# Kernel optimization log

Measured on AMD Instinct MI355X. Metric: run time of the kernel, lower is better.

## Reference

```python
import jax, jax.numpy as jnp
import numpy as np

BIT = 64
N_CLASS = 100
NUM_TRAIN = 100000
BATCH = 512
MU = 1.0   # config['mu']
M = 1.0    # config['m']
ETA = 0.5  # config['eta']
VUL = 1.0  # config['vul']
NTA = 1.0  # config['nta']


def setup_inputs() -> dict:
    key = jax.random.key(0)
    k1, k2, k3, k4, k5, k6 = jax.random.split(key, 6)
    u = jax.random.normal(k1, (BATCH, BIT), jnp.float32)
    # y / Y are one-hot label matrices in DFH; build realistic one-hot floats
    labels = jax.random.randint(k2, (BATCH,), 0, N_CLASS)
    y = jax.nn.one_hot(labels, N_CLASS, dtype=jnp.float32)
    ind = jax.random.randint(k3, (BATCH,), 0, NUM_TRAIN)
    U = jax.random.normal(k4, (BIT, NUM_TRAIN), jnp.float32)
    train_labels = jax.random.randint(k5, (NUM_TRAIN,), 0, N_CLASS)
    Y = jax.nn.one_hot(train_labels, N_CLASS, dtype=jnp.float32).T  # [n_class, num_train]
    V = jax.random.normal(k6, (BIT, N_CLASS), jnp.float32)
    return {"u": u, "y": y, "ind": ind, "U": U, "Y": Y, "V": V}


def _center_gradient(V, y, b):
    # 200-step gradient descent on V minimizing intra + vul*inter + nta*quant.
    n_class = V.shape[1]
    TK = V.shape[0] * (2.0 * jnp.eye(n_class, dtype=V.dtype)
                       - jnp.ones((n_class, n_class), V.dtype))
    yt = y.T  # [n_class, batch]

    def inner_loss(Vc):
        intra = jnp.mean((Vc @ yt - b) ** 2)
        inter = jnp.mean((Vc.T @ Vc - TK) ** 2)
        quant = jnp.mean((Vc - jnp.sign(Vc)) ** 2)
        return intra + VUL * inter + NTA * quant

    grad_fn = jax.grad(inner_loss)

    def step(Vc, i):
        # torch code multiplies alpha by 0.1 *before* the update at i==149 and i==179
        alpha = 0.03 * jnp.where(i >= 149, 0.1, 1.0) * jnp.where(i >= 179, 0.1, 1.0)
        return Vc - alpha * grad_fn(Vc), None

    V_new, _ = jax.lax.scan(step, V, jnp.arange(200))
    return V_new


def reference(u, y, ind, U, Y, V):
    # state buffer updates (torch: self.U[:, ind] = u.t().data, etc.)
    U = U.at[:, ind].set(u.T)
    Y = Y.at[:, ind].set(y.T)
    C = jnp.sign(V)
    b = jnp.sign(MU * (C @ y.T) + u.T)                     # [bit, batch]
    V_new = _center_gradient(V, y, b)                      # updated self.V
    s = (y @ Y > 0).astype(u.dtype)                        # [batch, num_train]
    ip = jnp.clip(0.5 * (u @ U), -100.0, 50.0)             # [batch, num_train]
    metric_loss = jnp.mean((1.0 - s) * jnp.log1p(jnp.exp(M + ip))
                           + s * jnp.log1p(jnp.exp(M - ip)))
    quantization_loss = jnp.mean((b - u.T) ** 2)
    loss = metric_loss + ETA * quantization_loss
    return loss, V_new
```

## Files before the change

kernel.cpp:

```cpp
#include <hip/hip_runtime.h>

#define BIT 64
#define NCLASS 100
#define NTRAIN 100000
#define BATCH 512

#define O_OWNER   0
#define O_TLAB    100000
#define O_LAB     200000
#define O_BMAT    200512
#define O_BSUM    233280
#define O_COUNT   239680
#define O_QSUM    239780
#define O_MSUM    239782

typedef __attribute__((ext_vector_type(8))) short short8v;
typedef __attribute__((ext_vector_type(4))) float f32x4;
typedef unsigned short ushortT;

__device__ __forceinline__ float signf(float x) {
    return (x > 0.f) ? 1.f : ((x < 0.f) ? -1.f : 0.f);
}

__device__ __forceinline__ ushortT f2bf(float x) {
    union { float f; unsigned u; } v; v.f = x;
    unsigned r = v.u + 0x7FFFu + ((v.u >> 16) & 1u);
    return (ushortT)(r >> 16);
}
__device__ __forceinline__ unsigned pk2(float a, float b) {
    return (unsigned)f2bf(a) | ((unsigned)f2bf(b) << 16);
}

__global__ void k_prep(const float* __restrict__ y, const int* __restrict__ ind,
                       int* owner, int* lab) {
    int b = threadIdx.x;
    const float* row = y + b * NCLASS;
    int best = 0;
    for (int c = 0; c < NCLASS; ++c)
        if (row[c] > 0.5f) best = c;
    lab[b] = best;
    atomicMax(&owner[ind[b]], b);
}

__global__ void k_tlab(const float* __restrict__ Y, const int* __restrict__ owner,
                       const int* __restrict__ lab, int* tlab) {
    int j = blockIdx.x * blockDim.x + threadIdx.x;
    if (j >= NTRAIN) return;
    int tl = 0;
    for (int c = 0; c < NCLASS; ++c)
        if (Y[(size_t)c * NTRAIN + j] > 0.5f) tl = c;
    int ow = owner[j];
    tlab[j] = (ow >= 0) ? lab[ow] : tl;
}

__global__ void k_b(const float* __restrict__ u, const float* __restrict__ V,
                    const int* __restrict__ lab, float* bmat, double* qsum) {
    int bb = threadIdx.x;
    int r  = blockIdx.x;
    int c = lab[bb];
    float v  = V[r * NCLASS + c];
    float uu = u[bb * BIT + r];
    float t  = signf(v) + uu;
    float bv = signf(t);
    bmat[r * BATCH + bb] = bv;
    float d = bv - uu;
    double q = (double)(d * d);
    for (int off = 32; off; off >>= 1) q += __shfl_down(q, off);
    __shared__ double wsum[8];
    int wid = threadIdx.x >> 6, lane = threadIdx.x & 63;
    if (lane == 0) wsum[wid] = q;
    __syncthreads();
    if (threadIdx.x == 0) {
        double s = 0;
        for (int w = 0; w < 8; ++w) s += wsum[w];
        atomicAdd(qsum, s);
    }
}

__global__ void k_bsum(const float* __restrict__ bmat, const int* __restrict__ lab,
                       float* Bsum, float* count) {
    __shared__ int slab[BATCH];
    for (int i = threadIdx.x; i < BATCH; i += blockDim.x) slab[i] = lab[i];
    __syncthreads();
    int idx = blockIdx.x * blockDim.x + threadIdx.x;
    if (idx < BIT * NCLASS) {
        int r = idx / NCLASS, c = idx % NCLASS;
        const float* br = bmat + r * BATCH;
        float s = 0.f;
        for (int bb = 0; bb < BATCH; ++bb)
            if (slab[bb] == c) s += br[bb];
        Bsum[idx] = s;
    }
    if (blockIdx.x == 0 && threadIdx.x < NCLASS) {
        int c = threadIdx.x, n = 0;
        for (int bb = 0; bb < BATCH; ++bb)
            if (slab[bb] == c) ++n;
        count[c] = (float)n;
    }
}

__global__ __launch_bounds__(512, 4) void k_main(
        const float* __restrict__ V, const float* __restrict__ Bsum,
        const float* __restrict__ count, const float* __restrict__ u,
        const float* __restrict__ U, const int* __restrict__ lab,
        const int* __restrict__ tlab, const int* __restrict__ owner,
        double* msum, float* __restrict__ out) {
    __shared__ __align__(16) char smem[69888];

    if (blockIdx.x == 0) {
        ushortT* SAb = (ushortT*)smem;
        ushortT* SBb = (ushortT*)(smem + 32768);
        ushortT* SMf = (ushortT*)(smem + 61440);
        float*   rs  = (float*)(smem + 69632);

        const int t = threadIdx.x, l = t & 63, w = t >> 6;
        const int g = l >> 4, c16 = l & 15;
        const short8v ONES = {0x3F80,0x3F80,0x3F80,0x3F80,
                              0x3F80,0x3F80,0x3F80,0x3F80};

        for (int i = t; i < 16384; i += 512) SAb[i] = 0;
        for (int i = t; i < 14336; i += 512) SBb[i] = 0;

        const float ci = 2.0f / 32768.0f;
        const float ce = 4.0f / 10000.0f;
        const float cq = 2.0f / 6400.0f;
        const float ce64 = 64.0f * ce;

        const int mtile = w & 3;
        const int m = mtile * 16 + c16;
        bool wact[4], live[4];
        int ntile[4], saO[4], sbO[4];
        float vreg[4][4], Kc[4][4], ncib[4][4];
        #pragma unroll
        for (int q = 0; q < 4; ++q) {
            const int tp = w + 8 * q;
            wact[q] = (tp < 28);
            const int nt = wact[q] ? (tp >> 2) : 0;
            ntile[q] = nt;
            const int n0 = nt * 16 + 4 * g;
            live[q] = wact[q] && (n0 < NCLASS);
            saO[q] = ((mtile * 4 + (nt >> 1)) * 64 + l) * 8 + 4 * (nt & 1);
            sbO[q] = ((nt * 2 + (mtile >> 1)) * 64 + (4 * g + 16 * (c16 >> 2))) * 8
                     + (c16 & 3) + 4 * (mtile & 1);
            #pragma unroll
            for (int r = 0; r < 4; ++r) {
                float v = 0.f, bs = 0.f, cn = 0.f;
                if (live[q]) {
                    const int n = n0 + r;
                    v  = V[m * NCLASS + n];
                    bs = Bsum[m * NCLASS + n];
                    cn = count[n];
                }
                vreg[q][r] = v;
                Kc[q][r]   = ci * cn + cq - 128.f * ce;
                ncib[q][r] = -ci * bs;
            }
        }

        const int mi_m = w >> 1, mj0 = (w & 1) * 2, mj1 = mj0 + 1;
        const bool dg = (mi_m == mj0) || (mi_m == mj1);
        const int smO0 = ((mj0 * 2 + (mi_m >> 1)) * 64 + l) * 8 + 4 * (mi_m & 1);
        const int smO1 = ((mj1 * 2 + (mi_m >> 1)) * 64 + l) * 8 + 4 * (mi_m & 1);

        __syncthreads();

        #pragma unroll
        for (int q = 0; q < 4; ++q) if (wact[q]) {
            *(uint2*)&SAb[saO[q]] =
                make_uint2(pk2(vreg[q][0], vreg[q][1]), pk2(vreg[q][2], vreg[q][3]));
            #pragma unroll
            for (int r = 0; r < 4; ++r) SBb[sbO[q] + r * 8] = f2bf(vreg[q][r]);
        }
        __syncthreads();

        int cur = 0;
        for (int step = 0; step < 200; ++step) {
            float alpha = 0.03f;
            if (step >= 149) alpha *= 0.1f;
            if (step >= 179) alpha *= 0.1f;

            const ushortT* SAc = SAb + cur * 8192;

            f32x4 aM0 = {0.f,0.f,0.f,0.f}, aM1 = {0.f,0.f,0.f,0.f};
            f32x4 aR  = {0.f,0.f,0.f,0.f};
            #pragma unroll
            for (int ks = 0; ks < 4; ++ks) {
                short8v a  = *(const short8v*)&SAc[((mi_m * 4 + ks) * 64 + l) * 8];
                short8v b0 = *(const short8v*)&SAc[((mj0 * 4 + ks) * 64 + l) * 8];
                short8v b1 = *(const short8v*)&SAc[((mj1 * 4 + ks) * 64 + l) * 8];
                aM0 = __builtin_amdgcn_mfma_f32_16x16x32_bf16(a, b0, aM0, 0, 0, 0);
                aM1 = __builtin_amdgcn_mfma_f32_16x16x32_bf16(a, b1, aM1, 0, 0, 0);
                if (dg)
                    aR = __builtin_amdgcn_mfma_f32_16x16x32_bf16(a, ONES, aR, 0, 0, 0);
            }
            *(uint2*)&SMf[smO0] = make_uint2(pk2(aM0[0], aM0[1]), pk2(aM0[2], aM0[3]));
            *(uint2*)&SMf[smO1] = make_uint2(pk2(aM1[0], aM1[1]), pk2(aM1[2], aM1[3]));
            if (dg && c16 == 0)
                *(f32x4*)&rs[mi_m * 16 + 4 * g] = aR;
            __syncthreads();

            const ushortT* SBc = SBb + cur * 7168;
            f32x4 p[4];
            #pragma unroll
            for (int q = 0; q < 4; ++q) p[q] = (f32x4){0.f,0.f,0.f,0.f};
            #pragma unroll
            for (int kb = 0; kb < 2; ++kb) {
                short8v bP = *(const short8v*)&SMf[((mtile * 2 + kb) * 64 + l) * 8];
                #pragma unroll
                for (int q = 0; q < 4; ++q) if (wact[q]) {
                    short8v aP = *(const short8v*)&SBc[((ntile[q] * 2 + kb) * 64 + l) * 8];
                    p[q] = __builtin_amdgcn_mfma_f32_16x16x32_bf16(aP, bP, p[q], 0, 0, 0);
                }
            }
            const float rsm = rs[m];

            const int nxt = cur ^ 1;
            ushortT* SAn = SAb + nxt * 8192;
            ushortT* SBn = SBb + nxt * 7168;
            #pragma unroll
            for (int q = 0; q < 4; ++q) if (wact[q]) {
                float nv[4];
                #pragma unroll
                for (int r = 0; r < 4; ++r) {
                    const float v = vreg[q][r];
                    float t1 = __builtin_fmaf(Kc[q][r], v, ncib[q][r]);
                    t1 = __builtin_fmaf(ce,   p[q][r], t1);
                    t1 = __builtin_fmaf(ce64, rsm,     t1);
                    t1 -= __builtin_copysignf(cq, v);
                    float vn = __builtin_fmaf(-alpha, t1, v);
                    vn = live[q] ? vn : 0.f;
                    vreg[q][r] = vn;
                    nv[r] = vn;
                }
                *(uint2*)&SAn[saO[q]] =
                    make_uint2(pk2(nv[0], nv[1]), pk2(nv[2], nv[3]));
                #pragma unroll
                for (int r = 0; r < 4; ++r) SBn[sbO[q] + r * 8] = f2bf(nv[r]);
            }
            __syncthreads();
            cur = nxt;
        }

        #pragma unroll
        for (int q = 0; q < 4; ++q) if (live[q]) {
            const int n0 = ntile[q] * 16 + 4 * g;
            #pragma unroll
            for (int r = 0; r < 4; ++r)
                out[1 + m * NCLASS + n0 + r] = vreg[q][r];
        }
    } else {
        float* ut   = (float*)smem;
        int*   slab = (int*)(smem + 34816);
        double* wsum = (double*)(smem + 36864);

        const int t = threadIdx.x;
        const int j = (blockIdx.x - 1) * 256 + (t & 255);
        const int half = t >> 8;
        slab[t] = lab[t];

        int tl = 0;
        const float* colbase = U;
        size_t cstride = NTRAIN;
        const bool jok = (j < NTRAIN);
        if (jok) {
            tl = tlab[j];
            int ow = owner[j];
            if (ow >= 0) { colbase = u + (size_t)ow * BIT; cstride = 1; }
            else         { colbase = U + j; }
        }

        float lsum = 0.f;
        for (int ci = 0; ci < 4; ++ci) {
            __syncthreads();
            for (int i = t; i < 8192; i += 512) {
                int buf = i >> 12, k = (i >> 6) & 63, r = i & 63;
                ut[buf * 4352 + r * 68 + k] = u[((buf * 4 + ci) * 64 + k) * BIT + r];
            }
            __syncthreads();

            if (jok) {
                const float* myut = ut + half * 4352;
                float acc[64];
                #pragma unroll
                for (int k = 0; k < 64; ++k) acc[k] = 0.f;
                #pragma unroll 2
                for (int r = 0; r < BIT; ++r) {
                    float Uv = colbase[(size_t)r * cstride];
                    const float* urow = &myut[r * 68];
                    #pragma unroll
                    for (int qq = 0; qq < 16; ++qq) {
                        float4 uv = *(const float4*)&urow[qq * 4];
                        acc[4 * qq + 0] += uv.x * Uv;
                        acc[4 * qq + 1] += uv.y * Uv;
                        acc[4 * qq + 2] += uv.z * Uv;
                        acc[4 * qq + 3] += uv.w * Uv;
                    }
                }
                const int b0 = (half * 4 + ci) * 64;
                #pragma unroll
                for (int k = 0; k < 64; ++k) {
                    float ip = fminf(fmaxf(0.5f * acc[k], -100.f), 50.f);
                    float x = (slab[b0 + k] == tl) ? (1.0f - ip) : (1.0f + ip);
                    lsum += fmaxf(x, 0.f) + __logf(1.f + __expf(-fabsf(x)));
                }
            }
        }

        double d = (double)lsum;
        for (int off = 32; off; off >>= 1) d += __shfl_down(d, off);
        const int wid = t >> 6, lane = t & 63;
        if (lane == 0) wsum[wid] = d;
        __syncthreads();
        if (t == 0) {
            double s = 0;
            for (int ww = 0; ww < 8; ++ww) s += wsum[ww];
            atomicAdd(msum, s);
        }
    }
}

__global__ void k_final(const double* __restrict__ msum,
                        const double* __restrict__ qsum, float* out) {
    if (threadIdx.x == 0) {
        double loss = (*msum) / ((double)BATCH * (double)NTRAIN)
                    + 0.5 * ((*qsum) / ((double)BIT * (double)BATCH));
        out[0] = (float)loss;
    }
}

extern "C" void kernel_launch(void* const* d_in, const int* in_sizes, int n_in,
                              void* d_out, int out_size, void* d_ws, size_t ws_size,
                              hipStream_t stream) {
    const float* u   = (const float*)d_in[0];
    const float* y   = (const float*)d_in[1];
    const int*   ind = (const int*)d_in[2];
    const float* U   = (const float*)d_in[3];
    const float* Y   = (const float*)d_in[4];
    const float* V   = (const float*)d_in[5];
    float* out = (float*)d_out;

    int*   wsI = (int*)d_ws;
    float* wsF = (float*)d_ws;
    int*   owner = wsI + O_OWNER;
    int*   tlab  = wsI + O_TLAB;
    int*   lab   = wsI + O_LAB;
    float* bmat  = wsF + O_BMAT;
    float* Bsum  = wsF + O_BSUM;
    float* count = wsF + O_COUNT;
    double* qsum = (double*)(wsF + O_QSUM);
    double* msum = (double*)(wsF + O_MSUM);

    hipMemsetAsync(owner, 0xFF, NTRAIN * sizeof(int), stream);
    hipMemsetAsync(wsF + O_QSUM, 0, 4 * sizeof(float), stream);

    k_prep<<<1, 512, 0, stream>>>(y, ind, owner, lab);
    k_tlab<<<(NTRAIN + 255) / 256, 256, 0, stream>>>(Y, owner, lab, tlab);
    k_b<<<64, 512, 0, stream>>>(u, V, lab, bmat, qsum);
    k_bsum<<<25, 256, 0, stream>>>(bmat, lab, Bsum, count);
    k_main<<<1 + (NTRAIN + 255) / 256, 512, 0, stream>>>(
        V, Bsum, count, u, U, lab, tlab, owner, msum, out);
    k_final<<<1, 64, 0, stream>>>(msum, qsum, out);
}
```

Before: 406.9 us.

## Fuse label decoding into main kernel and restructure center-gradient MFMA fragments

Drops the separate k_tlab launch: each metric block now decodes its train labels from the one-hot Y inside k_main (first half of the threads) and shares them through LDS. The center-gradient block reassigns MFMA tiles per wave, so each wave owns one m-tile and a contiguous group of n-tiles. Its bf16 conversions now use the hardware v_cvt_pk_bf16_f32 instruction instead of software rounding, and fragments are transposed with DPP lane swaps so they can be stored as packed vectors rather than scalar shorts. This removes a launch and the tlab round trip to global memory, and shortens the per-step serial latency of the 200-step loop. In exchange, each metric block pays a 100-load Y scan on half its threads before its GEMM work starts.

```diff
diff --git a/kernel.cpp b/kernel.cpp
--- a/kernel.cpp
+++ b/kernel.cpp
@@ -6,7 +6,6 @@
 #define BATCH 512
 
 #define O_OWNER   0
-#define O_TLAB    100000
 #define O_LAB     200000
 #define O_BMAT    200512
 #define O_BSUM    233280
@@ -22,13 +21,20 @@
     return (x > 0.f) ? 1.f : ((x < 0.f) ? -1.f : 0.f);
 }
 
-__device__ __forceinline__ ushortT f2bf(float x) {
-    union { float f; unsigned u; } v; v.f = x;
-    unsigned r = v.u + 0x7FFFu + ((v.u >> 16) & 1u);
-    return (ushortT)(r >> 16);
-}
-__device__ __forceinline__ unsigned pk2(float a, float b) {
-    return (unsigned)f2bf(a) | ((unsigned)f2bf(b) << 16);
+__device__ __forceinline__ unsigned cvtpk(float lo, float hi) {
+    unsigned r;
+    asm("v_cvt_pk_bf16_f32 %0, %1, %2" : "=v"(r) : "v"(lo), "v"(hi));
+    return r;
+}
+__device__ __forceinline__ float dpp_x1(float x) {
+    union { float f; int i; } v; v.f = x;
+    v.i = __builtin_amdgcn_mov_dpp(v.i, 0xB1, 0xF, 0xF, false);
+    return v.f;
+}
+__device__ __forceinline__ float dpp_x2(float x) {
+    union { float f; int i; } v; v.f = x;
+    v.i = __builtin_amdgcn_mov_dpp(v.i, 0x4E, 0xF, 0xF, false);
+    return v.f;
 }
 
 __global__ void k_prep(const float* __restrict__ y, const int* __restrict__ ind,
@@ -40,17 +46,6 @@
         if (row[c] > 0.5f) best = c;
     lab[b] = best;
     atomicMax(&owner[ind[b]], b);
-}
-
-__global__ void k_tlab(const float* __restrict__ Y, const int* __restrict__ owner,
-                       const int* __restrict__ lab, int* tlab) {
-    int j = blockIdx.x * blockDim.x + threadIdx.x;
-    if (j >= NTRAIN) return;
-    int tl = 0;
-    for (int c = 0; c < NCLASS; ++c)
-        if (Y[(size_t)c * NTRAIN + j] > 0.5f) tl = c;
-    int ow = owner[j];
-    tlab[j] = (ow >= 0) ? lab[ow] : tl;
 }
 
 __global__ void k_b(const float* __restrict__ u, const float* __restrict__ V,
@@ -102,8 +97,8 @@
 __global__ __launch_bounds__(512, 4) void k_main(
         const float* __restrict__ V, const float* __restrict__ Bsum,
         const float* __restrict__ count, const float* __restrict__ u,
-        const float* __restrict__ U, const int* __restrict__ lab,
-        const int* __restrict__ tlab, const int* __restrict__ owner,
+        const float* __restrict__ U, const float* __restrict__ Y,
+        const int* __restrict__ lab, const int* __restrict__ owner,
         double* msum, float* __restrict__ out) {
     __shared__ __align__(16) char smem[69888];
 
@@ -115,6 +110,10 @@
 
         const int t = threadIdx.x, l = t & 63, w = t >> 6;
         const int g = l >> 4, c16 = l & 15;
+        const int h = w >> 2;
+        const int mtile = w & 3;
+        const int m = mtile * 16 + c16;
+        const bool dg = ((mtile >> 1) == h);
         const short8v ONES = {0x3F80,0x3F80,0x3F80,0x3F80,
                               0x3F80,0x3F80,0x3F80,0x3F80};
 
@@ -126,22 +125,17 @@
         const float cq = 2.0f / 6400.0f;
         const float ce64 = 64.0f * ce;
 
-        const int mtile = w & 3;
-        const int m = mtile * 16 + c16;
-        bool wact[4], live[4];
-        int ntile[4], saO[4], sbO[4];
+        bool live[4];
+        int sbO[4];
         float vreg[4][4], Kc[4][4], ncib[4][4];
         #pragma unroll
         for (int q = 0; q < 4; ++q) {
-            const int tp = w + 8 * q;
-            wact[q] = (tp < 28);
-            const int nt = wact[q] ? (tp >> 2) : 0;
-            ntile[q] = nt;
+            const int nt = 4 * h + q;
             const int n0 = nt * 16 + 4 * g;
-            live[q] = wact[q] && (n0 < NCLASS);
-            saO[q] = ((mtile * 4 + (nt >> 1)) * 64 + l) * 8 + 4 * (nt & 1);
-            sbO[q] = ((nt * 2 + (mtile >> 1)) * 64 + (4 * g + 16 * (c16 >> 2))) * 8
-                     + (c16 & 3) + 4 * (mtile & 1);
+            const bool wact = (nt < 7);
+            live[q] = wact && (n0 < NCLASS);
+            sbO[q] = ((nt * 2 + (mtile >> 1)) * 64 +
+                      (16 * (c16 >> 2) + 4 * g + (c16 & 3))) * 8 + 4 * (mtile & 1);
             #pragma unroll
             for (int r = 0; r < 4; ++r) {
                 float v = 0.f, bs = 0.f, cn = 0.f;
@@ -156,21 +150,50 @@
                 ncib[q][r] = -ci * bs;
             }
         }
-
-        const int mi_m = w >> 1, mj0 = (w & 1) * 2, mj1 = mj0 + 1;
-        const bool dg = (mi_m == mj0) || (mi_m == mj1);
-        const int smO0 = ((mj0 * 2 + (mi_m >> 1)) * 64 + l) * 8 + 4 * (mi_m & 1);
-        const int smO1 = ((mj1 * 2 + (mi_m >> 1)) * 64 + l) * 8 + 4 * (mi_m & 1);
+        const int saO0 = (mtile * 4 + 2 * h) * 512 + l * 8;
+        const int saO1 = saO0 + 512;
+
+        auto store_frags = [&](ushortT* SAn, ushortT* SBn) {
+            uint4 wa;
+            wa.x = cvtpk(vreg[0][0], vreg[0][1]);
+            wa.y = cvtpk(vreg[0][2], vreg[0][3]);
+            wa.z = cvtpk(vreg[1][0], vreg[1][1]);
+            wa.w = cvtpk(vreg[1][2], vreg[1][3]);
+            *(uint4*)&SAn[saO0] = wa;
+            wa.x = cvtpk(vreg[2][0], vreg[2][1]);
+            wa.y = cvtpk(vreg[2][2], vreg[2][3]);
+            wa.z = cvtpk(vreg[3][0], vreg[3][1]);
+            wa.w = cvtpk(vreg[3][2], vreg[3][3]);
+            *(uint4*)&SAn[saO1] = wa;
+            #pragma unroll
+            for (int q = 0; q < 4; ++q) {
+                if (4 * h + q < 7) {
+                    float a0 = vreg[q][0], a1 = vreg[q][1];
+                    float a2 = vreg[q][2], a3 = vreg[q][3];
+                    float t0 = dpp_x1(a1), t1 = dpp_x1(a0);
+                    float t2 = dpp_x1(a3), t3 = dpp_x1(a2);
+                    const bool o1 = (l & 1);
+                    float c0 = o1 ? t0 : a0;
+                    float c1 = o1 ? a1 : t1;
+                    float c2 = o1 ? t2 : a2;
+                    float c3 = o1 ? a3 : t3;
+                    float u0 = dpp_x2(c2), u1 = dpp_x2(c3);
+                    float u2 = dpp_x2(c0), u3 = dpp_x2(c1);
+                    const bool o2 = (l & 2);
+                    float d0 = o2 ? u0 : c0;
+                    float d1 = o2 ? u1 : c1;
+                    float d2 = o2 ? c2 : u2;
+                    float d3 = o2 ? c3 : u3;
+                    uint2 wb;
+                    wb.x = cvtpk(d0, d1);
+                    wb.y = cvtpk(d2, d3);
+                    *(uint2*)&SBn[sbO[q]] = wb;
+                }
+            }
+        };
 
         __syncthreads();
-
-        #pragma unroll
-        for (int q = 0; q < 4; ++q) if (wact[q]) {
-            *(uint2*)&SAb[saO[q]] =
-                make_uint2(pk2(vreg[q][0], vreg[q][1]), pk2(vreg[q][2], vreg[q][3]));
-            #pragma unroll
-            for (int r = 0; r < 4; ++r) SBb[sbO[q] + r * 8] = f2bf(vreg[q][r]);
-        }
+        store_frags(SAb, SBb);
         __syncthreads();
 
         int cur = 0;
@@ -185,18 +208,24 @@
             f32x4 aR  = {0.f,0.f,0.f,0.f};
             #pragma unroll
             for (int ks = 0; ks < 4; ++ks) {
-                short8v a  = *(const short8v*)&SAc[((mi_m * 4 + ks) * 64 + l) * 8];
-                short8v b0 = *(const short8v*)&SAc[((mj0 * 4 + ks) * 64 + l) * 8];
-                short8v b1 = *(const short8v*)&SAc[((mj1 * 4 + ks) * 64 + l) * 8];
-                aM0 = __builtin_amdgcn_mfma_f32_16x16x32_bf16(a, b0, aM0, 0, 0, 0);
-                aM1 = __builtin_amdgcn_mfma_f32_16x16x32_bf16(a, b1, aM1, 0, 0, 0);
+                short8v b  = *(const short8v*)&SAc[mtile * 2048 + ks * 512 + l * 8];
+                short8v a0 = *(const short8v*)&SAc[(2 * h) * 2048 + ks * 512 + l * 8];
+                short8v a1 = *(const short8v*)&SAc[(2 * h + 1) * 2048 + ks * 512 + l * 8];
+                aM0 = __builtin_amdgcn_mfma_f32_16x16x32_bf16(a0, b, aM0, 0, 0, 0);
+                aM1 = __builtin_amdgcn_mfma_f32_16x16x32_bf16(a1, b, aM1, 0, 0, 0);
                 if (dg)
-                    aR = __builtin_amdgcn_mfma_f32_16x16x32_bf16(a, ONES, aR, 0, 0, 0);
-            }
-            *(uint2*)&SMf[smO0] = make_uint2(pk2(aM0[0], aM0[1]), pk2(aM0[2], aM0[3]));
-            *(uint2*)&SMf[smO1] = make_uint2(pk2(aM1[0], aM1[1]), pk2(aM1[2], aM1[3]));
+                    aR = __builtin_amdgcn_mfma_f32_16x16x32_bf16(b, ONES, aR, 0, 0, 0);
+            }
+            {
+                uint4 sm;
+                sm.x = cvtpk(aM0[0], aM0[1]);
+                sm.y = cvtpk(aM0[2], aM0[3]);
+                sm.z = cvtpk(aM1[0], aM1[1]);
+                sm.w = cvtpk(aM1[2], aM1[3]);
+                *(uint4*)&SMf[(mtile * 2 + h) * 512 + l * 8] = sm;
+            }
             if (dg && c16 == 0)
-                *(f32x4*)&rs[mi_m * 16 + 4 * g] = aR;
+                *(f32x4*)&rs[mtile * 16 + 4 * g] = aR;
             __syncthreads();
 
             const ushortT* SBc = SBb + cur * 7168;
@@ -205,76 +234,87 @@
             for (int q = 0; q < 4; ++q) p[q] = (f32x4){0.f,0.f,0.f,0.f};
             #pragma unroll
             for (int kb = 0; kb < 2; ++kb) {
-                short8v bP = *(const short8v*)&SMf[((mtile * 2 + kb) * 64 + l) * 8];
+                short8v bP = *(const short8v*)&SMf[(mtile * 2 + kb) * 512 + l * 8];
                 #pragma unroll
-                for (int q = 0; q < 4; ++q) if (wact[q]) {
-                    short8v aP = *(const short8v*)&SBc[((ntile[q] * 2 + kb) * 64 + l) * 8];
-                    p[q] = __builtin_amdgcn_mfma_f32_16x16x32_bf16(aP, bP, p[q], 0, 0, 0);
+                for (int q = 0; q < 4; ++q) {
+                    if (4 * h + q < 7) {
+                        short8v aP = *(const short8v*)
+                            &SBc[((4 * h + q) * 2 + kb) * 512 + l * 8];
+                        p[q] = __builtin_amdgcn_mfma_f32_16x16x32_bf16(aP, bP, p[q], 0, 0, 0);
+                    }
                 }
             }
             const float rsm = rs[m];
 
-            const int nxt = cur ^ 1;
-            ushortT* SAn = SAb + nxt * 8192;
-            ushortT* SBn = SBb + nxt * 7168;
-            #pragma unroll
-            for (int q = 0; q < 4; ++q) if (wact[q]) {
-                float nv[4];
+            #pragma unroll
+            for (int q = 0; q < 4; ++q) {
+                if (4 * h + q < 7) {
+                    #pragma unroll
+                    for (int r = 0; r < 4; ++r) {
+                        const float v = vreg[q][r];
+                        float t1 = __builtin_fmaf(Kc[q][r], v, ncib[q][r]);
+                        t1 = __builtin_fmaf(ce,   p[q][r], t1);
+                        t1 = __builtin_fmaf(ce64, rsm,     t1);
+                        t1 -= __builtin_copysignf(cq, v);
+                        float vn = __builtin_fmaf(-alpha, t1, v);
+                        vreg[q][r] = live[q] ? vn : 0.f;
+                    }
+                }
+            }
+            store_frags(SAb + (cur ^ 1) * 8192, SBb + (cur ^ 1) * 7168);
+            __syncthreads();
+            cur ^= 1;
+        }
+
+        #pragma unroll
+        for (int q = 0; q < 4; ++q) {
+            if (live[q]) {
+                const int n0 = (4 * h + q) * 16 + 4 * g;
                 #pragma unroll
-                for (int r = 0; r < 4; ++r) {
-                    const float v = vreg[q][r];
-                    float t1 = __builtin_fmaf(Kc[q][r], v, ncib[q][r]);
-                    t1 = __builtin_fmaf(ce,   p[q][r], t1);
-                    t1 = __builtin_fmaf(ce64, rsm,     t1);
-                    t1 -= __builtin_copysignf(cq, v);
-                    float vn = __builtin_fmaf(-alpha, t1, v);
-                    vn = live[q] ? vn : 0.f;
-                    vreg[q][r] = vn;
-                    nv[r] = vn;
-                }
-                *(uint2*)&SAn[saO[q]] =
-                    make_uint2(pk2(nv[0], nv[1]), pk2(nv[2], nv[3]));
-                #pragma unroll
-                for (int r = 0; r < 4; ++r) SBn[sbO[q] + r * 8] = f2bf(nv[r]);
-            }
-            __syncthreads();
-            cur = nxt;
-        }
-
-        #pragma unroll
-        for (int q = 0; q < 4; ++q) if (live[q]) {
-            const int n0 = ntile[q] * 16 + 4 * g;
-            #pragma unroll
-            for (int r = 0; r < 4; ++r)
-                out[1 + m * NCLASS + n0 + r] = vreg[q][r];
+                for (int r = 0; r < 4; ++r)
+                    out[1 + m * NCLASS + n0 + r] = vreg[q][r];
+            }
         }
     } else {
-        float* ut   = (float*)smem;
-        int*   slab = (int*)(smem + 34816);
+        float*  ut   = (float*)smem;
+        int*    slab = (int*)(smem + 34816);
         double* wsum = (double*)(smem + 36864);
+        int*    tls  = (int*)(smem + 36928);
 
         const int t = threadIdx.x;
-        const int j = (blockIdx.x - 1) * 256 + (t & 255);
+        const int jj = t & 255;
+        const int j = (blockIdx.x - 1) * 256 + jj;
         const int half = t >> 8;
+        const bool jok = (j < NTRAIN);
         slab[t] = lab[t];
 
-        int tl = 0;
+        if (half == 0) {
+            int tl = 0;
+            if (jok) {
+                for (int c = 0; c < NCLASS; ++c)
+                    if (Y[(size_t)c * NTRAIN + j] > 0.5f) tl = c;
+                int ow = owner[j];
+                if (ow >= 0) tl = lab[ow];
+            }
+            tls[jj] = tl;
+        }
+        __syncthreads();
+        const int tl = tls[jj];
+
         const float* colbase = U;
         size_t cstride = NTRAIN;
-        const bool jok = (j < NTRAIN);
         if (jok) {
-            tl = tlab[j];
             int ow = owner[j];
             if (ow >= 0) { colbase = u + (size_t)ow * BIT; cstride = 1; }
             else         { colbase = U + j; }
         }
 
         float lsum = 0.f;
-        for (int ci = 0; ci < 4; ++ci) {
+        for (int ch = 0; ch < 4; ++ch) {
             __syncthreads();
             for (int i = t; i < 8192; i += 512) {
                 int buf = i >> 12, k = (i >> 6) & 63, r = i & 63;
-                ut[buf * 4352 + r * 68 + k] = u[((buf * 4 + ci) * 64 + k) * BIT + r];
+                ut[buf * 4352 + r * 68 + k] = u[((buf * 4 + ch) * 64 + k) * BIT + r];
             }
             __syncthreads();
 
@@ -296,7 +336,7 @@
                         acc[4 * qq + 3] += uv.w * Uv;
                     }
                 }
-                const int b0 = (half * 4 + ci) * 64;
+                const int b0 = (half * 4 + ch) * 64;
                 #pragma unroll
                 for (int k = 0; k < 64; ++k) {
                     float ip = fminf(fmaxf(0.5f * acc[k], -100.f), 50.f);
@@ -342,7 +382,6 @@
     int*   wsI = (int*)d_ws;
     float* wsF = (float*)d_ws;
     int*   owner = wsI + O_OWNER;
-    int*   tlab  = wsI + O_TLAB;
     int*   lab   = wsI + O_LAB;
     float* bmat  = wsF + O_BMAT;
     float* Bsum  = wsF + O_BSUM;
@@ -354,10 +393,9 @@
     hipMemsetAsync(wsF + O_QSUM, 0, 4 * sizeof(float), stream);
 
     k_prep<<<1, 512, 0, stream>>>(y, ind, owner, lab);
-    k_tlab<<<(NTRAIN + 255) / 256, 256, 0, stream>>>(Y, owner, lab, tlab);
     k_b<<<64, 512, 0, stream>>>(u, V, lab, bmat, qsum);
     k_bsum<<<25, 256, 0, stream>>>(bmat, lab, Bsum, count);
     k_main<<<1 + (NTRAIN + 255) / 256, 512, 0, stream>>>(
-        V, Bsum, count, u, U, lab, tlab, owner, msum, out);
+        V, Bsum, count, u, U, Y, lab, owner, msum, out);
     k_final<<<1, 64, 0, stream>>>(msum, qsum, out);
 }
```

After: 392.3 us. 1.04x faster.
